# Optimization experiments

Hardware: AMD Instinct MI355X
Metric: run time of the kernel (lower is better)

## Reference

```python
import jax, jax.numpy as jnp
import numpy as np

A = 3          # num agents (hardcoded in original forward)
AF = 3         # features per agent


def gru_cell(xt, h, Wih, Whh, bih, bhh):
    # PyTorch GRU cell math. xt: (B, Din), h: (B, H)
    gi = xt @ Wih.T + bih            # (B, 3H)
    gh = h @ Whh.T + bhh             # (B, 3H)
    i_r, i_z, i_n = jnp.split(gi, 3, axis=-1)
    h_r, h_z, h_n = jnp.split(gh, 3, axis=-1)
    r = jax.nn.sigmoid(i_r + h_r)
    z = jax.nn.sigmoid(i_z + h_z)
    n = jnp.tanh(i_n + r * h_n)
    return (1.0 - z) * n + z * h


def setup_inputs() -> dict:
    key = jax.random.key(0)
    ks = jax.random.split(key, 20)
    B, T, H, OUT = 1024, 256, 256, 9
    s = 0.05
    inp = {
        "x": jax.random.normal(ks[0], (B, T, A * AF), dtype=jnp.float32),
        # agent attention
        "Wa": jax.random.normal(ks[1], (H, AF), dtype=jnp.float32) * s,
        "ba": jnp.zeros((H,), dtype=jnp.float32),
        "va": jax.random.normal(ks[2], (H,), dtype=jnp.float32) * s,
        # encoder GRU (input dim = AF = 3)
        "enc_Wih": jax.random.normal(ks[3], (3 * H, AF), dtype=jnp.float32) * s,
        "enc_Whh": jax.random.normal(ks[4], (3 * H, H), dtype=jnp.float32) * s,
        "enc_bih": jnp.zeros((3 * H,), dtype=jnp.float32),
        "enc_bhh": jnp.zeros((3 * H,), dtype=jnp.float32),
        # decoder GRU (input dim = OUT + H)
        "dec_Wih": jax.random.normal(ks[5], (3 * H, OUT + H), dtype=jnp.float32) * s,
        "dec_Whh": jax.random.normal(ks[6], (3 * H, H), dtype=jnp.float32) * s,
        "dec_bih": jnp.zeros((3 * H,), dtype=jnp.float32),
        "dec_bhh": jnp.zeros((3 * H,), dtype=jnp.float32),
        # temporal (Bahdanau) attention
        "Wt": jax.random.normal(ks[7], (H, 2 * H), dtype=jnp.float32) * s,
        "bt": jnp.zeros((H,), dtype=jnp.float32),
        "vt": jax.random.normal(ks[8], (H,), dtype=jnp.float32) * s,
        # output projection
        "Wfc": jax.random.normal(ks[9], (OUT, H), dtype=jnp.float32) * s,
        "bfc": jnp.zeros((OUT,), dtype=jnp.float32),
        "pred_len": 16,
    }
    return inp


def reference(x, Wa, ba, va, enc_Wih, enc_Whh, enc_bih, enc_bhh,
              dec_Wih, dec_Whh, dec_bih, dec_bhh, Wt, bt, vt, Wfc, bfc,
              pred_len):
    B, T, _ = x.shape
    H = Wa.shape[0]
    x_agents = x.reshape(B, T, A, AF)

    # --- agent attention, vectorized over all timesteps ---
    energy = jnp.tanh(jnp.einsum('btaf,hf->btah', x_agents, Wa) + ba)  # (B,T,A,H)
    scores = jnp.einsum('btah,h->bta', energy, va)                      # (B,T,A)
    aw = jax.nn.softmax(scores, axis=-1)
    timestep_reprs = jnp.einsum('bta,btaf->btf', aw, x_agents)          # (B,T,AF)

    # --- encoder GRU over T via scan ---
    h0 = jnp.zeros((B, H), dtype=x.dtype)

    def enc_step(h, xt):
        h_new = gru_cell(xt, h, enc_Wih, enc_Whh, enc_bih, enc_bhh)
        return h_new, h_new

    h_enc, enc_out_t = jax.lax.scan(enc_step, h0, jnp.swapaxes(timestep_reprs, 0, 1))
    encoder_outputs = jnp.swapaxes(enc_out_t, 0, 1)  # (B,T,H)

    # precompute encoder half of temporal attention energy: Wt = [Wt_dec | Wt_enc]
    Wt_dec, Wt_enc = Wt[:, :H], Wt[:, H:]
    enc_proj = jnp.einsum('bth,gh->btg', encoder_outputs, Wt_enc)  # (B,T,H)

    # --- decoder loop via scan ---
    def dec_step(carry, _):
        h, dec_in = carry                                  # h: (B,H), dec_in: (B,OUT)
        e = jnp.tanh(enc_proj + (h @ Wt_dec.T + bt)[:, None, :])   # (B,T,H)
        tscore = jnp.einsum('bth,h->bt', e, vt)
        tw = jax.nn.softmax(tscore, axis=-1)
        context = jnp.einsum('bt,bth->bh', tw, encoder_outputs)
        inp = jnp.concatenate([dec_in, context], axis=-1)          # (B, OUT+H)
        h_new = gru_cell(inp, h, dec_Wih, dec_Whh, dec_bih, dec_bhh)
        pred = h_new @ Wfc.T + bfc                                 # (B, OUT)
        return (h_new, pred), pred

    init = (h_enc, x[:, -1, :])
    _, preds = jax.lax.scan(dec_step, init, None, length=pred_len)  # (P,B,OUT)
    outputs = jnp.swapaxes(preds, 0, 1)                             # (B,P,OUT)
    return outputs.reshape(-1, outputs.shape[-1])
```

## Files before the change

kernel.cpp:

```cpp
#include <hip/hip_runtime.h>
#include <hip/hip_bf16.h>

typedef __hip_bfloat16 bf16;
typedef __attribute__((ext_vector_type(8))) short s16x8;
typedef __attribute__((ext_vector_type(4))) float f32x4;
typedef __attribute__((ext_vector_type(2))) float f32x2;

#define B_TOT 1024
#define T_LEN 256
#define H_DIM 256
#define PRED_LEN 16

__device__ __forceinline__ float b2f(short u) {
  union { unsigned int i; float f; } c;
  c.i = ((unsigned int)(unsigned short)u) << 16;
  return c.f;
}
__device__ __forceinline__ float fsig(float x) {
  return __builtin_amdgcn_rcpf(1.f + __expf(-x));
}
__device__ __forceinline__ float ftanh(float x) {
  return 1.f - 2.f * __builtin_amdgcn_rcpf(1.f + __expf(2.f * x));
}
__device__ __forceinline__ f32x4 mfma16(s16x8 a, s16x8 b, f32x4 c) {
  return __builtin_amdgcn_mfma_f32_16x16x32_bf16(a, b, c, 0, 0, 0);
}
template <int HI>
__device__ __forceinline__ f32x2 fp8pk2f(unsigned int pk) {
  return __builtin_amdgcn_cvt_pk_f32_fp8(pk, HI);
}
__device__ __forceinline__ unsigned char f2fp8(float v) {
  return (unsigned char)(__builtin_amdgcn_cvt_pk_fp8_f32(v, v, 0, 0) & 0xff);
}
__device__ __forceinline__ uint2 pk8fp8(s16x8 hv) {
  unsigned int lo = 0, hi = 0;
  lo = __builtin_amdgcn_cvt_pk_fp8_f32(b2f(hv[0]), b2f(hv[1]), lo, 0);
  lo = __builtin_amdgcn_cvt_pk_fp8_f32(b2f(hv[2]), b2f(hv[3]), lo, 1);
  hi = __builtin_amdgcn_cvt_pk_fp8_f32(b2f(hv[4]), b2f(hv[5]), hi, 0);
  hi = __builtin_amdgcn_cvt_pk_fp8_f32(b2f(hv[6]), b2f(hv[7]), hi, 1);
  uint2 w; w.x = lo; w.y = hi; return w;
}

__global__ __launch_bounds__(256) void convert_kernel(
    const float* __restrict__ eWhh, const float* __restrict__ Wt,
    const float* __restrict__ dWhh, const float* __restrict__ dWih,
    bf16* __restrict__ encWF, bf16* __restrict__ wtEncF,
    bf16* __restrict__ wtDec, bf16* __restrict__ whhD, bf16* __restrict__ wihPD)
{
  int i = blockIdx.x*256 + threadIdx.x;
  if (i < 24576) {
    int l = i & 63, kc = (i>>6)&7, tile = i>>9;
    int j = tile*16 + (l&15);
    int k = kc*32 + ((l>>4)&3)*8;
    #pragma unroll
    for (int e = 0; e < 8; ++e)
      encWF[i*8+e] = __float2bfloat16(eWhh[j*256 + k + e]);
  } else if (i < 32768) {
    int s = i - 24576;
    int l = s & 63, kc = (s>>6)&7, tile = s>>9;
    int j = tile*16 + (l&15);
    int k = kc*32 + ((l>>4)&3)*8;
    #pragma unroll
    for (int e = 0; e < 8; ++e)
      wtEncF[s*8+e] = __float2bfloat16(Wt[j*512 + 256 + k + e]);
  }
  if (i < 768*288) {
    int g = i / 288, k = i - g*288;
    wihPD[i] = __float2bfloat16((k < 265) ? dWih[g*265 + k] : 0.f);
  }
  if (i < 256*256) {
    int g = i >> 8, k = i & 255;
    wtDec[i] = __float2bfloat16(Wt[g*512 + k]);
  }
  if (i < 768*256) whhD[i] = __float2bfloat16(dWhh[i]);
}

__global__ __launch_bounds__(256) void agent_attn_kernel(
    const float* __restrict__ x, const float* __restrict__ Wa,
    const float* __restrict__ ba, const float* __restrict__ va,
    float* __restrict__ treprs)
{
  __shared__ float w0[256], w1[256], w2[256], baL[256], vaL[256];
  int tid = threadIdx.x;
  w0[tid] = Wa[tid*3+0];
  w1[tid] = Wa[tid*3+1];
  w2[tid] = Wa[tid*3+2];
  baL[tid] = ba[tid];
  vaL[tid] = va[tid];
  __syncthreads();
  long idx = (long)blockIdx.x * 256 + tid;
  float xa[9];
  #pragma unroll
  for (int i = 0; i < 9; ++i) xa[i] = x[idx*9 + i];
  float s0 = 0.f, s1 = 0.f, s2 = 0.f;
  for (int h = 0; h < 256; ++h) {
    float a0 = w0[h], a1 = w1[h], a2 = w2[h], bb = baL[h], vv = vaL[h];
    s0 += ftanh(a0*xa[0] + a1*xa[1] + a2*xa[2] + bb) * vv;
    s1 += ftanh(a0*xa[3] + a1*xa[4] + a2*xa[5] + bb) * vv;
    s2 += ftanh(a0*xa[6] + a1*xa[7] + a2*xa[8] + bb) * vv;
  }
  float mx = fmaxf(s0, fmaxf(s1, s2));
  float e0 = __expf(s0-mx), e1 = __expf(s1-mx), e2 = __expf(s2-mx);
  float inv = __builtin_amdgcn_rcpf(e0+e1+e2);
  e0 *= inv; e1 *= inv; e2 *= inv;
  treprs[idx*3+0] = e0*xa[0] + e1*xa[3] + e2*xa[6];
  treprs[idx*3+1] = e0*xa[1] + e1*xa[4] + e2*xa[7];
  treprs[idx*3+2] = e0*xa[2] + e1*xa[5] + e2*xa[8];
}

__global__ __launch_bounds__(512, 2) void encoder_kernel(
    const bf16* __restrict__ encWF, const float* __restrict__ eWih,
    const float* __restrict__ ebih, const float* __restrict__ ebhh,
    const float* __restrict__ treprs, unsigned char* __restrict__ eo8,
    float* __restrict__ h_enc)
{
  __shared__ __align__(16) bf16  hbF[8*64*8];
  __shared__ __align__(16) bf16  hb_lin[4*264];
  __shared__ __align__(16) float hf[4*260];
  __shared__ __align__(16) f32x4 wihAll[768];
  __shared__ float bhhnL[256];
  __shared__ float xtL[2][16];

  const int tid = threadIdx.x;
  const int b0 = blockIdx.x * 4;

  for (int i = tid; i < 768; i += 512) {
    f32x4 w;
    w.x = eWih[i*3+0]; w.y = eWih[i*3+1]; w.z = eWih[i*3+2];
    w.w = (i < 512) ? (ebih[i] + ebhh[i]) : ebih[i];
    wihAll[i] = w;
    if (i >= 512) bhhnL[i-512] = ebhh[i];
  }
  for (int i = tid; i < 4*260; i += 512) hf[i] = 0.f;
  for (int i = tid; i < 8*64*8; i += 512) hbF[i] = __float2bfloat16(0.f);
  for (int i = tid; i < 4*264; i += 512) hb_lin[i] = __float2bfloat16(0.f);
  if (tid < 16) {
    int b = tid >> 2, f = tid & 3;
    xtL[0][tid] = (f < 3) ? treprs[((long)(b0+b)*T_LEN + 0)*3 + f] : 0.f;
  }

  const int lane = tid & 63;
  const int wv   = tid >> 6;
  const int nrow = lane & 15;
  const int quad = lane >> 4;

  s16x8 wf[32];
  #pragma unroll
  for (int u = 0; u < 4; ++u) {
    int tile = (u < 2) ? (2*wv + u) : (16 + 2*wv + (u-2));
    #pragma unroll
    for (int kc = 0; kc < 8; ++kc)
      wf[u*8+kc] = *(const s16x8*)(encWF + (((long)tile*8 + kc)*64 + lane)*8);
  }
  __syncthreads();

  for (int t = 0; t < 256; ++t) {
    s16x8 afr[8];
    #pragma unroll
    for (int kc = 0; kc < 8; ++kc)
      afr[kc] = *(const s16x8*)&hbF[(kc*64 + lane)*8];
    if (t >= 1 && tid < 128) {
      int b = tid >> 5, seg = tid & 31;
      s16x8 hv = *(const s16x8*)&hb_lin[b*264 + seg*8];
      *(uint2*)(eo8 + ((long)(b0+b)*T_LEN + (t-1))*H_DIM + seg*8) = pk8fp8(hv);
    }
    __syncthreads();

    f32x4 acc[6] = {};
    #pragma unroll
    for (int kc = 0; kc < 8; ++kc) {
      #pragma unroll
      for (int u = 0; u < 4; ++u)
        acc[u] = mfma16(afr[kc], wf[u*8+kc], acc[u]);
    }
    #pragma unroll
    for (int half = 0; half < 2; ++half) {
      s16x8 nf[8];
      #pragma unroll
      for (int kc = 0; kc < 8; ++kc)
        nf[kc] = *(const s16x8*)(encWF + (((long)(32 + 2*wv + half)*8 + kc)*64 + lane)*8);
      #pragma unroll
      for (int kc = 0; kc < 8; ++kc)
        acc[4+half] = mfma16(afr[kc], nf[kc], acc[4+half]);
    }

    if (t < 255 && tid < 16) {
      int b = tid >> 2, f = tid & 3;
      xtL[(t+1)&1][tid] = (f < 3) ? treprs[((long)(b0+b)*T_LEN + (t+1))*3 + f] : 0.f;
    }

    {
      float x0 = xtL[t & 1][quad*4+0];
      float x1 = xtL[t & 1][quad*4+1];
      float x2 = xtL[t & 1][quad*4+2];
      #pragma unroll
      for (int c = 0; c < 2; ++c) {
        int j = wv*32 + c*16 + nrow;
        f32x4 wr = wihAll[j];
        f32x4 wz = wihAll[256+j];
        f32x4 wn = wihAll[512+j];
        float rg = fsig(wr.x*x0 + wr.y*x1 + wr.z*x2 + wr.w + acc[c][0]);
        float zg = fsig(wz.x*x0 + wz.y*x1 + wz.z*x2 + wz.w + acc[2+c][0]);
        float ng = ftanh(wn.x*x0 + wn.y*x1 + wn.z*x2 + wn.w
                         + rg*(acc[4+c][0] + bhhnL[j]));
        float hold = hf[quad*260 + j];
        float hnew = ng + zg*(hold - ng);
        hf[quad*260 + j] = hnew;
        bf16 hv = __float2bfloat16(hnew);
        hb_lin[quad*264 + j] = hv;
        hbF[((j>>5)*64 + ((j>>3)&3)*16 + 4*quad)*8 + (j&7)] = hv;
      }
    }
    __syncthreads();
  }

  if (tid < 128) {
    int b = tid >> 5, seg = tid & 31;
    s16x8 hv = *(const s16x8*)&hb_lin[b*264 + seg*8];
    *(uint2*)(eo8 + ((long)(b0+b)*T_LEN + 255)*H_DIM + seg*8) = pk8fp8(hv);
  }
  for (int i = tid; i < 4*256; i += 512) {
    int m = i >> 8, j = i & 255;
    h_enc[(long)(b0+m)*H_DIM + j] = hf[m*260 + j];
  }
}

__global__ __launch_bounds__(256) void proj_kernel(
    const unsigned char* __restrict__ eo8, const bf16* __restrict__ wtEncF,
    unsigned char* __restrict__ ep8)
{
  __shared__ __align__(16) bf16 Asm[4*8*64*8];
  __shared__ __align__(16) unsigned char Cst[64*256];
  const int tid = threadIdx.x;
  const long R0 = (long)blockIdx.x * 64;
  const int lane = tid & 63, wv = tid >> 6;
  const int nrow = lane & 15, quad = lane >> 4;

  #pragma unroll
  for (int s8 = 0; s8 < 8; ++s8) {
    int s = tid + s8*256;
    int l = s & 63, kc = (s>>6)&7, at = s>>9;
    int m = at*16 + (l&15), k = kc*32 + ((l>>4)&3)*8;
    uint2 v = *(const uint2*)(eo8 + (R0+m)*H_DIM + k);
    s16x8 o; f32x2 d;
    d = fp8pk2f<0>(v.x); o[0] = __bfloat16_as_short(__float2bfloat16(d.x)); o[1] = __bfloat16_as_short(__float2bfloat16(d.y));
    d = fp8pk2f<1>(v.x); o[2] = __bfloat16_as_short(__float2bfloat16(d.x)); o[3] = __bfloat16_as_short(__float2bfloat16(d.y));
    d = fp8pk2f<0>(v.y); o[4] = __bfloat16_as_short(__float2bfloat16(d.x)); o[5] = __bfloat16_as_short(__float2bfloat16(d.y));
    d = fp8pk2f<1>(v.y); o[6] = __bfloat16_as_short(__float2bfloat16(d.x)); o[7] = __bfloat16_as_short(__float2bfloat16(d.y));
    *(s16x8*)&Asm[s*8] = o;
  }
  __syncthreads();

  f32x4 acc[16];
  #pragma unroll
  for (int n = 0; n < 16; ++n) acc[n] = f32x4{0.f,0.f,0.f,0.f};
  #pragma unroll
  for (int kc = 0; kc < 8; ++kc) {
    s16x8 a = *(const s16x8*)&Asm[((wv*8 + kc)*64 + lane)*8];
    #pragma unroll
    for (int nt = 0; nt < 16; ++nt) {
      s16x8 b = *(const s16x8*)(wtEncF + ((nt*8 + kc)*64 + lane)*8);
      acc[nt] = mfma16(a, b, acc[nt]);
    }
  }
  #pragma unroll
  for (int nt = 0; nt < 16; ++nt)
    #pragma unroll
    for (int r = 0; r < 4; ++r)
      Cst[(wv*16 + quad*4 + r)*256 + nt*16 + nrow] = f2fp8(acc[nt][r]);
  __syncthreads();

  {
    int row = tid >> 2, seg = tid & 3;
    #pragma unroll
    for (int p = 0; p < 4; ++p)
      *(uint4*)(ep8 + (R0+row)*H_DIM + seg*64 + p*16) =
          *(const uint4*)&Cst[row*256 + seg*64 + p*16];
  }
}

__global__ __launch_bounds__(512, 4) void decoder_kernel(
    const float* __restrict__ x, const bf16* __restrict__ wtDec,
    const float* __restrict__ bt, const float* __restrict__ vt,
    const bf16* __restrict__ wihPD, const bf16* __restrict__ whhD,
    const float* __restrict__ dbih, const float* __restrict__ dbhh,
    const float* __restrict__ Wfc, const float* __restrict__ bfc,
    const unsigned char* __restrict__ eo8, const unsigned char* __restrict__ ep8,
    const float* __restrict__ h_enc, float* __restrict__ out)
{
  __shared__ __align__(16) float hfL[2*260];
  __shared__ __align__(16) bf16  hbL[16*264];
  __shared__ __align__(16) float qL[2*260];
  __shared__ float twL[2*260];
  __shared__ __align__(16) bf16  inpb[16*296];
  __shared__ __align__(16) float vtL[256];
  __shared__ float btL[256];
  __shared__ float bsumL[512];
  __shared__ float bihnL[256];
  __shared__ float bhhnL[256];
  __shared__ float ghL[6*260];
  __shared__ __align__(16) float WfcL[9*260];
  __shared__ float bfcL[9];
  __shared__ float decin[24];
  __shared__ __align__(16) float scratch[4096];

  const int tid = threadIdx.x;
  const int b0 = blockIdx.x * 2;

  for (int i = tid; i < 256; i += 512) {
    vtL[i] = vt[i]; btL[i] = bt[i];
    bihnL[i] = dbih[512+i]; bhhnL[i] = dbhh[512+i];
  }
  if (tid < 512) bsumL[tid] = dbih[tid] + dbhh[tid];
  for (int i = tid; i < 9*256; i += 512) { int o = i >> 8, k = i & 255; WfcL[o*260+k] = Wfc[i]; }
  if (tid < 9) bfcL[tid] = bfc[tid];
  for (int i = tid; i < 2*260; i += 512) { int m = i/260, j = i - m*260; hfL[i] = (j < 256) ? h_enc[(long)(b0+m)*H_DIM + j] : 0.f; }
  for (int i = tid; i < 16*264; i += 512) {
    int m = i/264, j = i - m*264;
    hbL[i] = (m < 2 && j < 256) ? __float2bfloat16(h_enc[(long)(b0+m)*H_DIM + j])
                                : __float2bfloat16(0.f);
  }
  for (int i = tid; i < 16*296; i += 512) inpb[i] = __float2bfloat16(0.f);
  if (tid < 18) { int b = tid/9, o = tid - b*9; decin[b*12+o] = x[((long)(b0+b)*T_LEN + (T_LEN-1))*9 + o]; }
  __syncthreads();

  const int lane = tid & 63;
  const int wv   = tid >> 6;
  const int nrow = lane & 15;
  const int quad = lane >> 4;
  const int jr0  = wv*16 + nrow;

  for (int s = 0; s < PRED_LEN; ++s) {
    #pragma unroll 1
    for (int half = 0; half < 2; ++half) {
      const int j = jr0 + half*128;
      f32x4 qa = {}, ghr = {}, ghz = {}, ghn = {};
      #pragma unroll
      for (int kc = 0; kc < 8; ++kc) {
        s16x8 a = *(const s16x8*)&hbL[nrow*264 + kc*32 + quad*8];
        qa  = mfma16(a, *(const s16x8*)(wtDec + (long)j*256 + kc*32 + quad*8), qa);
        ghr = mfma16(a, *(const s16x8*)(whhD + (long)j*256 + kc*32 + quad*8), ghr);
        ghz = mfma16(a, *(const s16x8*)(whhD + (long)(256+j)*256 + kc*32 + quad*8), ghz);
        ghn = mfma16(a, *(const s16x8*)(whhD + (long)(512+j)*256 + kc*32 + quad*8), ghn);
      }
      if (quad == 0) {
        #pragma unroll
        for (int r = 0; r < 2; ++r) {
          qL[r*260 + j]       = qa[r] + btL[j];
          ghL[(0+r)*260 + j]  = ghr[r];
          ghL[(2+r)*260 + j]  = ghz[r];
          ghL[(4+r)*260 + j]  = ghn[r];
        }
      }
    }
    __syncthreads();

    {
      int bb = tid >> 8, t = tid & 255;
      const float* qrow = &qL[bb*260];
      const uint4* ep4 = (const uint4*)(ep8 + ((long)(b0+bb)*T_LEN + t)*H_DIM);
      float s0 = 0.f, s1 = 0.f;
      #pragma unroll 4
      for (int kc = 0; kc < 16; ++kc) {
        uint4 pv = ep4[kc];
        int k = kc*16;
        f32x2 d;
        d = fp8pk2f<0>(pv.x); s0 += ftanh(d.x + qrow[k+0])*vtL[k+0];  s1 += ftanh(d.y + qrow[k+1])*vtL[k+1];
        d = fp8pk2f<1>(pv.x); s0 += ftanh(d.x + qrow[k+2])*vtL[k+2];  s1 += ftanh(d.y + qrow[k+3])*vtL[k+3];
        d = fp8pk2f<0>(pv.y); s0 += ftanh(d.x + qrow[k+4])*vtL[k+4];  s1 += ftanh(d.y + qrow[k+5])*vtL[k+5];
        d = fp8pk2f<1>(pv.y); s0 += ftanh(d.x + qrow[k+6])*vtL[k+6];  s1 += ftanh(d.y + qrow[k+7])*vtL[k+7];
        d = fp8pk2f<0>(pv.z); s0 += ftanh(d.x + qrow[k+8])*vtL[k+8];  s1 += ftanh(d.y + qrow[k+9])*vtL[k+9];
        d = fp8pk2f<1>(pv.z); s0 += ftanh(d.x + qrow[k+10])*vtL[k+10]; s1 += ftanh(d.y + qrow[k+11])*vtL[k+11];
        d = fp8pk2f<0>(pv.w); s0 += ftanh(d.x + qrow[k+12])*vtL[k+12]; s1 += ftanh(d.y + qrow[k+13])*vtL[k+13];
        d = fp8pk2f<1>(pv.w); s0 += ftanh(d.x + qrow[k+14])*vtL[k+14]; s1 += ftanh(d.y + qrow[k+15])*vtL[k+15];
      }
      scratch[bb*256 + t] = s0 + s1;
    }
    __syncthreads();

    if (wv < 2) {
      float v4[4];
      float mx = -1e30f;
      #pragma unroll
      for (int i = 0; i < 4; ++i) { v4[i] = scratch[wv*256 + lane + 64*i]; mx = fmaxf(mx, v4[i]); }
      #pragma unroll
      for (int off = 1; off < 64; off <<= 1) mx = fmaxf(mx, __shfl_xor(mx, off));
      float sum = 0.f;
      #pragma unroll
      for (int i = 0; i < 4; ++i) { v4[i] = __expf(v4[i] - mx); sum += v4[i]; }
      #pragma unroll
      for (int off = 1; off < 64; off <<= 1) sum += __shfl_xor(sum, off);
      float inv = __builtin_amdgcn_rcpf(sum);
      #pragma unroll
      for (int i = 0; i < 4; ++i) twL[wv*260 + lane + 64*i] = v4[i] * inv;
    }
    __syncthreads();

    {
      int tq = wv;
      int b = lane >> 5, h8 = (lane & 31) * 8;
      const unsigned char* eob = eo8 + ((long)(b0+b)*T_LEN + tq*32)*H_DIM + h8;
      const float* tw = &twL[b*260 + tq*32];
      float c[8] = {};
      #pragma unroll 8
      for (int t = 0; t < 32; ++t) {
        uint2 ev = *(const uint2*)(eob + (long)t*H_DIM);
        float w = tw[t];
        f32x2 d0 = fp8pk2f<0>(ev.x);
        f32x2 d1 = fp8pk2f<1>(ev.x);
        f32x2 d2 = fp8pk2f<0>(ev.y);
        f32x2 d3 = fp8pk2f<1>(ev.y);
        c[0] += w*d0.x; c[1] += w*d0.y; c[2] += w*d1.x; c[3] += w*d1.y;
        c[4] += w*d2.x; c[5] += w*d2.y; c[6] += w*d3.x; c[7] += w*d3.y;
      }
      f32x4 cc0; cc0.x = c[0]; cc0.y = c[1]; cc0.z = c[2]; cc0.w = c[3];
      f32x4 cc1; cc1.x = c[4]; cc1.y = c[5]; cc1.z = c[6]; cc1.w = c[7];
      *(f32x4*)&scratch[tq*512 + b*256 + h8 + 0] = cc0;
      *(f32x4*)&scratch[tq*512 + b*256 + h8 + 4] = cc1;
    }
    __syncthreads();

    {
      int b = tid >> 8, h = tid & 255;
      float sum = 0.f;
      #pragma unroll
      for (int tq = 0; tq < 8; ++tq) sum += scratch[tq*512 + b*256 + h];
      inpb[b*296 + 9 + h] = __float2bfloat16(sum);
    }
    if (tid < 18) {
      int bb = tid/9, o = tid - bb*9;
      inpb[bb*296 + o] = __float2bfloat16(decin[bb*12 + o]);
    }
    __syncthreads();

    #pragma unroll 1
    for (int half = 0; half < 2; ++half) {
      const int j = jr0 + half*128;
      f32x4 gir = {}, giz = {}, gin = {};
      #pragma unroll
      for (int kc = 0; kc < 9; ++kc) {
        s16x8 a = *(const s16x8*)&inpb[nrow*296 + kc*32 + quad*8];
        gir = mfma16(a, *(const s16x8*)(wihPD + (long)j*288 + kc*32 + quad*8), gir);
        giz = mfma16(a, *(const s16x8*)(wihPD + (long)(256+j)*288 + kc*32 + quad*8), giz);
        gin = mfma16(a, *(const s16x8*)(wihPD + (long)(512+j)*288 + kc*32 + quad*8), gin);
      }
      if (quad == 0) {
        #pragma unroll
        for (int r = 0; r < 2; ++r) {
          float rg = fsig(gir[r] + ghL[(0+r)*260 + j] + bsumL[j]);
          float zg = fsig(giz[r] + ghL[(2+r)*260 + j] + bsumL[256+j]);
          float ng = ftanh(gin[r] + bihnL[j] + rg*(ghL[(4+r)*260 + j] + bhhnL[j]));
          float hold = hfL[r*260 + j];
          float hnew = ng + zg*(hold - ng);
          hfL[r*260 + j] = hnew;
          hbL[r*264 + j] = __float2bfloat16(hnew);
        }
      }
    }
    __syncthreads();

    if (tid < 144) {
      int b = tid / 72, rem = tid - b*72;
      int o = rem >> 3, ch = rem & 7;
      float ps = 0.f;
      #pragma unroll
      for (int k = ch*32; k < ch*32 + 32; ++k)
        ps += hfL[b*260 + k] * WfcL[o*260 + k];
      scratch[tid] = ps;
    }
    __syncthreads();
    if (tid < 18) {
      int b = tid / 9, o = tid - b*9;
      float sum = bfcL[o];
      #pragma unroll
      for (int ch = 0; ch < 8; ++ch) sum += scratch[b*72 + o*8 + ch];
      out[((long)(b0+b)*PRED_LEN + s)*9 + o] = sum;
      decin[b*12 + o] = sum;
    }
    __syncthreads();
  }
}

extern "C" void kernel_launch(void* const* d_in, const int* in_sizes, int n_in,
                              void* d_out, int out_size, void* d_ws, size_t ws_size,
                              hipStream_t stream)
{
  const float* x    = (const float*)d_in[0];
  const float* Wa   = (const float*)d_in[1];
  const float* ba   = (const float*)d_in[2];
  const float* va   = (const float*)d_in[3];
  const float* eWih = (const float*)d_in[4];
  const float* eWhh = (const float*)d_in[5];
  const float* ebih = (const float*)d_in[6];
  const float* ebhh = (const float*)d_in[7];
  const float* dWih = (const float*)d_in[8];
  const float* dWhh = (const float*)d_in[9];
  const float* dbih = (const float*)d_in[10];
  const float* dbhh = (const float*)d_in[11];
  const float* Wt   = (const float*)d_in[12];
  const float* bt   = (const float*)d_in[13];
  const float* vt   = (const float*)d_in[14];
  const float* Wfc  = (const float*)d_in[15];
  const float* bfc  = (const float*)d_in[16];
  float* out = (float*)d_out;

  char* ws = (char*)d_ws;
  size_t off = 0;
  bf16* encWF   = (bf16*)(ws + off); off += (size_t)48*8*64*8*sizeof(bf16);
  bf16* wtEncF  = (bf16*)(ws + off); off += (size_t)16*8*64*8*sizeof(bf16);
  bf16* wtDec   = (bf16*)(ws + off); off += (size_t)256*256*sizeof(bf16);
  bf16* whhD    = (bf16*)(ws + off); off += (size_t)768*256*sizeof(bf16);
  bf16* wihPD   = (bf16*)(ws + off); off += (size_t)768*288*sizeof(bf16);
  float* treprs = (float*)(ws + off); off += (size_t)B_TOT*T_LEN*3*sizeof(float);
  float* h_enc  = (float*)(ws + off); off += (size_t)B_TOT*H_DIM*sizeof(float);
  unsigned char* eo8 = (unsigned char*)(ws + off); off += (size_t)B_TOT*T_LEN*H_DIM;
  unsigned char* ep8 = (unsigned char*)(ws + off); off += (size_t)B_TOT*T_LEN*H_DIM;

  if (ws_size < off) return;

  convert_kernel<<<(768*288 + 255)/256, 256, 0, stream>>>(
      eWhh, Wt, dWhh, dWih, encWF, wtEncF, wtDec, whhD, wihPD);
  agent_attn_kernel<<<B_TOT*T_LEN/256, 256, 0, stream>>>(x, Wa, ba, va, treprs);
  encoder_kernel<<<B_TOT/4, 512, 0, stream>>>(encWF, eWih, ebih, ebhh,
                                              treprs, eo8, h_enc);
  proj_kernel<<<B_TOT*T_LEN/64, 256, 0, stream>>>(eo8, wtEncF, ep8);
  decoder_kernel<<<B_TOT/2, 512, 0, stream>>>(x, wtDec, bt, vt, wihPD, whhD,
                                              dbih, dbhh, Wfc, bfc, eo8, ep8,
                                              h_enc, out);
}
```

Before: 1.637 ms.

## Remap attention score loop so lanes split H and read contiguous fp8 rows

```diff
diff --git a/kernel.cpp b/kernel.cpp
--- a/kernel.cpp
+++ b/kernel.cpp
@@ -290,10 +290,10 @@
 {
   __shared__ __align__(16) float hfL[2*260];
   __shared__ __align__(16) bf16  hbL[16*264];
-  __shared__ __align__(16) float qL[2*260];
+  __shared__ __align__(16) float qP[2*276];
+  __shared__ __align__(16) float vtP[276];
   __shared__ float twL[2*260];
   __shared__ __align__(16) bf16  inpb[16*296];
-  __shared__ __align__(16) float vtL[256];
   __shared__ float btL[256];
   __shared__ float bsumL[512];
   __shared__ float bihnL[256];
@@ -308,7 +308,8 @@
   const int b0 = blockIdx.x * 2;
 
   for (int i = tid; i < 256; i += 512) {
-    vtL[i] = vt[i]; btL[i] = bt[i];
+    vtP[(i>>4)*17 + (i&15)] = vt[i];
+    btL[i] = bt[i];
     bihnL[i] = dbih[512+i]; bhhnL[i] = dbhh[512+i];
   }
   if (tid < 512) bsumL[tid] = dbih[tid] + dbhh[tid];
@@ -346,7 +347,7 @@
       if (quad == 0) {
         #pragma unroll
         for (int r = 0; r < 2; ++r) {
-          qL[r*260 + j]       = qa[r] + btL[j];
+          qP[r*276 + (j>>4)*17 + (j&15)] = qa[r] + btL[j];
           ghL[(0+r)*260 + j]  = ghr[r];
           ghL[(2+r)*260 + j]  = ghz[r];
           ghL[(4+r)*260 + j]  = ghn[r];
@@ -356,25 +357,31 @@
     __syncthreads();
 
     {
-      int bb = tid >> 8, t = tid & 255;
-      const float* qrow = &qL[bb*260];
-      const uint4* ep4 = (const uint4*)(ep8 + ((long)(b0+bb)*T_LEN + t)*H_DIM);
-      float s0 = 0.f, s1 = 0.f;
-      #pragma unroll 4
-      for (int kc = 0; kc < 16; ++kc) {
-        uint4 pv = ep4[kc];
-        int k = kc*16;
+      int b = wv >> 2, w4 = wv & 3;
+      int kc = lane & 15, tr = lane >> 4;
+      const float* qp = &qP[b*276];
+      const unsigned char* epb =
+          ep8 + ((long)(b0+b)*T_LEN + w4*64)*H_DIM + kc*16;
+      const int k = kc*17;
+      #pragma unroll 2
+      for (int i = 0; i < 16; ++i) {
+        int t4 = i*4 + tr;
+        uint4 pv = *(const uint4*)(epb + (long)t4*H_DIM);
+        float s0 = 0.f, s1 = 0.f;
         f32x2 d;
-        d = fp8pk2f<0>(pv.x); s0 += ftanh(d.x + qrow[k+0])*vtL[k+0];  s1 += ftanh(d.y + qrow[k+1])*vtL[k+1];
-        d = fp8pk2f<1>(pv.x); s0 += ftanh(d.x + qrow[k+2])*vtL[k+2];  s1 += ftanh(d.y + qrow[k+3])*vtL[k+3];
-        d = fp8pk2f<0>(pv.y); s0 += ftanh(d.x + qrow[k+4])*vtL[k+4];  s1 += ftanh(d.y + qrow[k+5])*vtL[k+5];
-        d = fp8pk2f<1>(pv.y); s0 += ftanh(d.x + qrow[k+6])*vtL[k+6];  s1 += ftanh(d.y + qrow[k+7])*vtL[k+7];
-        d = fp8pk2f<0>(pv.z); s0 += ftanh(d.x + qrow[k+8])*vtL[k+8];  s1 += ftanh(d.y + qrow[k+9])*vtL[k+9];
-        d = fp8pk2f<1>(pv.z); s0 += ftanh(d.x + qrow[k+10])*vtL[k+10]; s1 += ftanh(d.y + qrow[k+11])*vtL[k+11];
-        d = fp8pk2f<0>(pv.w); s0 += ftanh(d.x + qrow[k+12])*vtL[k+12]; s1 += ftanh(d.y + qrow[k+13])*vtL[k+13];
-        d = fp8pk2f<1>(pv.w); s0 += ftanh(d.x + qrow[k+14])*vtL[k+14]; s1 += ftanh(d.y + qrow[k+15])*vtL[k+15];
-      }
-      scratch[bb*256 + t] = s0 + s1;
+        d = fp8pk2f<0>(pv.x); s0 += ftanh(d.x + qp[k+0])*vtP[k+0];   s1 += ftanh(d.y + qp[k+1])*vtP[k+1];
+        d = fp8pk2f<1>(pv.x); s0 += ftanh(d.x + qp[k+2])*vtP[k+2];   s1 += ftanh(d.y + qp[k+3])*vtP[k+3];
+        d = fp8pk2f<0>(pv.y); s0 += ftanh(d.x + qp[k+4])*vtP[k+4];   s1 += ftanh(d.y + qp[k+5])*vtP[k+5];
+        d = fp8pk2f<1>(pv.y); s0 += ftanh(d.x + qp[k+6])*vtP[k+6];   s1 += ftanh(d.y + qp[k+7])*vtP[k+7];
+        d = fp8pk2f<0>(pv.z); s0 += ftanh(d.x + qp[k+8])*vtP[k+8];   s1 += ftanh(d.y + qp[k+9])*vtP[k+9];
+        d = fp8pk2f<1>(pv.z); s0 += ftanh(d.x + qp[k+10])*vtP[k+10]; s1 += ftanh(d.y + qp[k+11])*vtP[k+11];
+        d = fp8pk2f<0>(pv.w); s0 += ftanh(d.x + qp[k+12])*vtP[k+12]; s1 += ftanh(d.y + qp[k+13])*vtP[k+13];
+        d = fp8pk2f<1>(pv.w); s0 += ftanh(d.x + qp[k+14])*vtP[k+14]; s1 += ftanh(d.y + qp[k+15])*vtP[k+15];
+        float sc = s0 + s1;
+        #pragma unroll
+        for (int off = 1; off < 16; off <<= 1) sc += __shfl_xor(sc, off);
+        if (kc == 0) scratch[b*256 + w4*64 + t4] = sc;
+      }
     }
     __syncthreads();
 
```

Result: faster. 1.574 ms (-3.9%).
